# Kernel optimization log

Hardware: AMD Instinct MI355X
Metric: run time of the kernel (lower is better)

Reference implementation:

```python
import jax, jax.numpy as jnp
import numpy as np

INPUT_SIZE = 2048
MEM_SIZE = 4096


def setup_inputs() -> dict:
    key = jax.random.key(0)
    ks = jax.random.split(key, 16)
    u = lambda k, s: jax.random.uniform(k, s, dtype=jnp.float32)
    inp = {
        "x": jax.random.normal(ks[0], (1, INPUT_SIZE), dtype=jnp.float32),
        "h0": jnp.zeros((1, MEM_SIZE), jnp.float32),
        "c0": jnp.zeros((1, MEM_SIZE), jnp.float32),
        "w_inpgate": u(ks[1], (INPUT_SIZE, MEM_SIZE)),
        "w_rec_inpgate": u(ks[2], (MEM_SIZE, MEM_SIZE)),
        "w_mem_inpgate": u(ks[3], (MEM_SIZE, MEM_SIZE)),
        "w_inp": jnp.ones((INPUT_SIZE, MEM_SIZE), jnp.float32),
        "w_rec_inp": jnp.ones((MEM_SIZE, MEM_SIZE), jnp.float32),
        "w_forgetgate": u(ks[4], (INPUT_SIZE, MEM_SIZE)),
        "w_rec_forgetgate": u(ks[5], (MEM_SIZE, MEM_SIZE)),
        "w_mem_forgetgate": u(ks[6], (MEM_SIZE, MEM_SIZE)),
        "w_outgate": u(ks[7], (INPUT_SIZE, MEM_SIZE)),
        "w_rec_outgate": u(ks[8], (MEM_SIZE, MEM_SIZE)),
        "w_mem_outgate": u(ks[9], (MEM_SIZE, MEM_SIZE)),
        "w_hid_out": u(ks[10], (MEM_SIZE, 1)),
        "b_inpgate": u(ks[11], (1, MEM_SIZE)),
        "b_inp": u(ks[12], (1, MEM_SIZE)),
        "b_forgetgate": u(ks[13], (1, MEM_SIZE)),
        "b_outgate": u(ks[14], (1, MEM_SIZE)),
        "is_reset": 1,
    }
    return inp


def reference(x, h0, c0,
              w_inpgate, w_rec_inpgate, w_mem_inpgate,
              w_inp, w_rec_inp,
              w_forgetgate, w_rec_forgetgate, w_mem_forgetgate,
              w_outgate, w_rec_outgate, w_mem_outgate,
              w_hid_out,
              b_inpgate, b_inp, b_forgetgate, b_outgate,
              is_reset):
    # is_reset is a static Python int (matches module's reset() semantics)
    if is_reset:
        h = jnp.zeros_like(h0)
        c = jnp.zeros_like(c0)
    else:
        h, c = h0, c0
    # Fused-GEMM form of the 11 tiny matmuls: concat weights along gate axis.
    Wx = jnp.concatenate([w_inpgate, w_forgetgate, w_outgate, w_inp], axis=1)      # [I, 4M]
    Wh = jnp.concatenate([w_rec_inpgate, w_rec_forgetgate, w_rec_outgate, w_rec_inp], axis=1)  # [M, 4M]
    Wc = jnp.concatenate([w_mem_inpgate, w_mem_forgetgate, w_mem_outgate], axis=1)  # [M, 3M]
    b = jnp.concatenate([b_inpgate, b_forgetgate, b_outgate, b_inp], axis=1)        # [1, 4M]
    z = x @ Wx + h @ Wh + b                      # [1, 4M]
    zc = c @ Wc                                   # [1, 3M]
    M = h.shape[1]
    z = z.at[:, : 3 * M].add(zc)
    inp_gate = jax.nn.sigmoid(z[:, 0:M])
    forget_gate = jax.nn.sigmoid(z[:, M:2 * M])
    out_gate = jax.nn.sigmoid(z[:, 2 * M:3 * M])
    ct_new = jnp.tanh(z[:, 3 * M:4 * M])
    c_t = inp_gate * ct_new + forget_gate * c     # [1, M]
    h_t = out_gate * jnp.tanh(c_t)                # [1, M]
    # Module returns w_hid_out.mm(h): (M,1) @ (1,M) outer product -> (M, M)
    out = w_hid_out @ h_t
    return out
```

## Files before the change

### kernel.cpp

```cpp
#include <hip/hip_runtime.h>
#include <math.h>

#define MSZ 4096
#define ISZ 2048
#define NSPLIT 64
#define KC (ISZ / NSPLIT)

typedef float fx4 __attribute__((ext_vector_type(4)));

__global__ __launch_bounds__(256, 3) void k_matvec(
    const float* __restrict__ x,
    const float* __restrict__ w_inpgate,
    const float* __restrict__ w_outgate,
    const float* __restrict__ w_inp,
    float* __restrict__ z_part)
{
    const int b       = blockIdx.x;
    const int gate    = b / (4 * NSPLIT);
    const int rem     = b % (4 * NSPLIT);
    const int coltile = rem / NSPLIT;
    const int split   = rem % NSPLIT;

    const float* W = (gate == 0) ? w_inpgate : (gate == 1) ? w_outgate : w_inp;
    const fx4* W4  = (const fx4*)W + (size_t)split * KC * (MSZ / 4);

    const int c4 = coltile * 256 + threadIdx.x;

    float xr[KC];
    #pragma unroll
    for (int i = 0; i < KC; ++i) xr[i] = x[split * KC + i];

    fx4 acc0 = {0.f, 0.f, 0.f, 0.f};
    fx4 acc1 = {0.f, 0.f, 0.f, 0.f};
    #pragma unroll
    for (int ii = 0; ii < KC; ii += 2) {
        acc0 += xr[ii]     * W4[(size_t)(ii)     * (MSZ / 4) + c4];
        acc1 += xr[ii + 1] * W4[(size_t)(ii + 1) * (MSZ / 4) + c4];
    }
    ((fx4*)z_part)[((size_t)split * 3 + gate) * (MSZ / 4) + c4] = acc0 + acc1;
}

__global__ __launch_bounds__(256) void k_act(
    const float* __restrict__ z_part,
    const float* __restrict__ b_inpgate,
    const float* __restrict__ b_outgate,
    const float* __restrict__ b_inp,
    float* __restrict__ h_t)
{
    const int j = blockIdx.x * 256 + threadIdx.x;
    float zi0 = b_inpgate[j], zi1 = 0.f;
    float zo0 = b_outgate[j], zo1 = 0.f;
    float zc0 = b_inp[j],     zc1 = 0.f;
    #pragma unroll 8
    for (int s = 0; s < NSPLIT; s += 2) {
        const float* zp0 = z_part + (size_t)(s)     * 3 * MSZ;
        const float* zp1 = z_part + (size_t)(s + 1) * 3 * MSZ;
        zi0 += zp0[0 * MSZ + j];  zi1 += zp1[0 * MSZ + j];
        zo0 += zp0[1 * MSZ + j];  zo1 += zp1[1 * MSZ + j];
        zc0 += zp0[2 * MSZ + j];  zc1 += zp1[2 * MSZ + j];
    }
    const float zi = zi0 + zi1, zo = zo0 + zo1, zc = zc0 + zc1;
    const float ig  = 1.f / (1.f + __expf(-zi));
    const float og  = 1.f / (1.f + __expf(-zo));
    const float ct  = tanhf(zc);
    const float c_t = ig * ct;
    h_t[j] = og * tanhf(c_t);
}

#define CBLK 2048
__global__ __launch_bounds__(256) void k_outer(
    const float* __restrict__ w_hid_out,
    const float* __restrict__ h_t,
    fx4* __restrict__ out4)
{
    const fx4* h4 = (const fx4*)h_t;
    int i = blockIdx.x * 256 + threadIdx.x;
    #pragma unroll
    for (int it = 0; it < (MSZ * (MSZ / 4)) / (CBLK * 256); ++it, i += CBLK * 256) {
        const int row = i >> 10;
        const float w = w_hid_out[row];
        const fx4 o = w * h4[i & 1023];
        __builtin_nontemporal_store(o, &out4[i]);
    }
}

extern "C" void kernel_launch(void* const* d_in, const int* in_sizes, int n_in,
                              void* d_out, int out_size, void* d_ws, size_t ws_size,
                              hipStream_t stream) {
    const float* x          = (const float*)d_in[0];
    const float* w_inpgate  = (const float*)d_in[3];
    const float* w_inp      = (const float*)d_in[6];
    const float* w_outgate  = (const float*)d_in[11];
    const float* w_hid_out  = (const float*)d_in[14];
    const float* b_inpgate  = (const float*)d_in[15];
    const float* b_inp      = (const float*)d_in[16];
    const float* b_outgate  = (const float*)d_in[18];

    float* z_part = (float*)d_ws;
    float* h_t    = z_part + (size_t)NSPLIT * 3 * MSZ;

    k_matvec<<<3 * 4 * NSPLIT, 256, 0, stream>>>(x, w_inpgate, w_outgate, w_inp, z_part);
    k_act<<<MSZ / 256, 256, 0, stream>>>(z_part, b_inpgate, b_outgate, b_inp, h_t);
    k_outer<<<CBLK, 256, 0, stream>>>(w_hid_out, h_t, (fx4*)d_out);
}
```

Baseline: 440.6 us.

## Fuse gate matvec, activation and outer product into one column-tiled kernel

Replaces the three-kernel pipeline (split-K matvec, partial-sum reduction plus activation, outer-product writer) with a single kernel. Each block owns 16 output columns. It reduces over all input rows within the block using shuffles and shared memory, computes h_t for those columns, and then writes those columns of the outer product for every row. This removes the z_part workspace round trip and two kernel launches. In exchange, weight reads and output stores become 64-byte strided segments rather than fully contiguous rows, and the launch is limited to 256 blocks of 512 threads, which may reduce occupancy.

```diff
diff --git a/kernel.cpp b/kernel.cpp
--- a/kernel.cpp
+++ b/kernel.cpp
@@ -3,84 +3,101 @@
 
 #define MSZ 4096
 #define ISZ 2048
-#define NSPLIT 64
-#define KC (ISZ / NSPLIT)
+#define NB   256
+#define NT   512
+#define NCOLS 16
+#define ROWLANES 128
+#define RITER (ISZ / ROWLANES)
+#define OITER (MSZ / ROWLANES)
 
 typedef float fx4 __attribute__((ext_vector_type(4)));
 
-__global__ __launch_bounds__(256, 3) void k_matvec(
+__global__ __launch_bounds__(NT) void k_lstm(
     const float* __restrict__ x,
     const float* __restrict__ w_inpgate,
     const float* __restrict__ w_outgate,
     const float* __restrict__ w_inp,
-    float* __restrict__ z_part)
-{
-    const int b       = blockIdx.x;
-    const int gate    = b / (4 * NSPLIT);
-    const int rem     = b % (4 * NSPLIT);
-    const int coltile = rem / NSPLIT;
-    const int split   = rem % NSPLIT;
-
-    const float* W = (gate == 0) ? w_inpgate : (gate == 1) ? w_outgate : w_inp;
-    const fx4* W4  = (const fx4*)W + (size_t)split * KC * (MSZ / 4);
-
-    const int c4 = coltile * 256 + threadIdx.x;
-
-    float xr[KC];
-    #pragma unroll
-    for (int i = 0; i < KC; ++i) xr[i] = x[split * KC + i];
-
-    fx4 acc0 = {0.f, 0.f, 0.f, 0.f};
-    fx4 acc1 = {0.f, 0.f, 0.f, 0.f};
-    #pragma unroll
-    for (int ii = 0; ii < KC; ii += 2) {
-        acc0 += xr[ii]     * W4[(size_t)(ii)     * (MSZ / 4) + c4];
-        acc1 += xr[ii + 1] * W4[(size_t)(ii + 1) * (MSZ / 4) + c4];
-    }
-    ((fx4*)z_part)[((size_t)split * 3 + gate) * (MSZ / 4) + c4] = acc0 + acc1;
-}
-
-__global__ __launch_bounds__(256) void k_act(
-    const float* __restrict__ z_part,
     const float* __restrict__ b_inpgate,
     const float* __restrict__ b_outgate,
     const float* __restrict__ b_inp,
-    float* __restrict__ h_t)
-{
-    const int j = blockIdx.x * 256 + threadIdx.x;
-    float zi0 = b_inpgate[j], zi1 = 0.f;
-    float zo0 = b_outgate[j], zo1 = 0.f;
-    float zc0 = b_inp[j],     zc1 = 0.f;
-    #pragma unroll 8
-    for (int s = 0; s < NSPLIT; s += 2) {
-        const float* zp0 = z_part + (size_t)(s)     * 3 * MSZ;
-        const float* zp1 = z_part + (size_t)(s + 1) * 3 * MSZ;
-        zi0 += zp0[0 * MSZ + j];  zi1 += zp1[0 * MSZ + j];
-        zo0 += zp0[1 * MSZ + j];  zo1 += zp1[1 * MSZ + j];
-        zc0 += zp0[2 * MSZ + j];  zc1 += zp1[2 * MSZ + j];
-    }
-    const float zi = zi0 + zi1, zo = zo0 + zo1, zc = zc0 + zc1;
-    const float ig  = 1.f / (1.f + __expf(-zi));
-    const float og  = 1.f / (1.f + __expf(-zo));
-    const float ct  = tanhf(zc);
-    const float c_t = ig * ct;
-    h_t[j] = og * tanhf(c_t);
-}
-
-#define CBLK 2048
-__global__ __launch_bounds__(256) void k_outer(
     const float* __restrict__ w_hid_out,
-    const float* __restrict__ h_t,
     fx4* __restrict__ out4)
 {
-    const fx4* h4 = (const fx4*)h_t;
-    int i = blockIdx.x * 256 + threadIdx.x;
+    const int b    = blockIdx.x;
+    const int t    = threadIdx.x;
+    const int cg   = t & 3;
+    const int rl   = t >> 2;
+    const int wave = t >> 6;
+    const int lane = t & 63;
+    const int jbase = b * NCOLS;
+    const int c4    = (jbase >> 2) + cg;
+
+    __shared__ float red[3][8][4][4];
+    __shared__ fx4   hsh4[4];
+
+    float xr[RITER];
     #pragma unroll
-    for (int it = 0; it < (MSZ * (MSZ / 4)) / (CBLK * 256); ++it, i += CBLK * 256) {
-        const int row = i >> 10;
+    for (int i = 0; i < RITER; ++i) xr[i] = x[rl + ROWLANES * i];
+
+    const float* Wg[3] = {w_inpgate, w_outgate, w_inp};
+
+    #pragma unroll
+    for (int g = 0; g < 3; ++g) {
+        const fx4* W4 = (const fx4*)Wg[g];
+        fx4 w[RITER];
+        #pragma unroll
+        for (int i = 0; i < RITER; ++i)
+            w[i] = W4[(size_t)(rl + ROWLANES * i) * (MSZ / 4) + c4];
+
+        fx4 a0 = {0.f, 0.f, 0.f, 0.f};
+        fx4 a1 = {0.f, 0.f, 0.f, 0.f};
+        #pragma unroll
+        for (int i = 0; i < RITER; i += 2) {
+            a0 += xr[i]     * w[i];
+            a1 += xr[i + 1] * w[i + 1];
+        }
+        fx4 acc = a0 + a1;
+
+        #pragma unroll
+        for (int s = 4; s <= 32; s <<= 1) {
+            acc.x += __shfl_xor(acc.x, s);
+            acc.y += __shfl_xor(acc.y, s);
+            acc.z += __shfl_xor(acc.z, s);
+            acc.w += __shfl_xor(acc.w, s);
+        }
+        if (lane < 4) {
+            red[g][wave][lane][0] = acc.x;
+            red[g][wave][lane][1] = acc.y;
+            red[g][wave][lane][2] = acc.z;
+            red[g][wave][lane][3] = acc.w;
+        }
+    }
+    __syncthreads();
+
+    if (t < NCOLS) {
+        const int g4 = t >> 2, el = t & 3;
+        float zi = b_inpgate[jbase + t];
+        float zo = b_outgate[jbase + t];
+        float zc = b_inp[jbase + t];
+        #pragma unroll
+        for (int wv = 0; wv < 8; ++wv) {
+            zi += red[0][wv][g4][el];
+            zo += red[1][wv][g4][el];
+            zc += red[2][wv][g4][el];
+        }
+        const float ig  = 1.f / (1.f + __expf(-zi));
+        const float og  = 1.f / (1.f + __expf(-zo));
+        const float ct  = tanhf(zc);
+        ((float*)hsh4)[t] = og * tanhf(ig * ct);
+    }
+    __syncthreads();
+
+    const fx4 hv = hsh4[cg];
+    #pragma unroll 8
+    for (int i = 0; i < OITER; ++i) {
+        const int row = rl + ROWLANES * i;
         const float w = w_hid_out[row];
-        const fx4 o = w * h4[i & 1023];
-        __builtin_nontemporal_store(o, &out4[i]);
+        __builtin_nontemporal_store(w * hv, &out4[(size_t)row * (MSZ / 4) + c4]);
     }
 }
 
@@ -96,10 +113,7 @@
     const float* b_inp      = (const float*)d_in[16];
     const float* b_outgate  = (const float*)d_in[18];
 
-    float* z_part = (float*)d_ws;
-    float* h_t    = z_part + (size_t)NSPLIT * 3 * MSZ;
-
-    k_matvec<<<3 * 4 * NSPLIT, 256, 0, stream>>>(x, w_inpgate, w_outgate, w_inp, z_part);
-    k_act<<<MSZ / 256, 256, 0, stream>>>(z_part, b_inpgate, b_outgate, b_inp, h_t);
-    k_outer<<<CBLK, 256, 0, stream>>>(w_hid_out, h_t, (fx4*)d_out);
+    k_lstm<<<NB, NT, 0, stream>>>(x, w_inpgate, w_outgate, w_inp,
+                                  b_inpgate, b_outgate, b_inp,
+                                  w_hid_out, (fx4*)d_out);
 }
```

After: 441.7 us. About the same (+0.3%).
